# Optimization experiments

Measured on AMD Instinct MI355X. Metric: run time of the kernel, lower is better.

Reference implementation:

```python
import jax, jax.numpy as jnp
import numpy as np

B, S, D, H = 4, 4096, 1024, 16
DH = D // H  # 64
EPS = 1e-6


def setup_inputs() -> dict:
    key = jax.random.key(0)
    ks = jax.random.split(key, 6)
    scale = 1.0 / np.sqrt(D).astype(np.float32)
    x = jax.random.normal(ks[0], (B, S, D), jnp.float32)
    # packed cache: rows 0..DH-1 = KV state S0, row DH = normalizer z0 (kept positive)
    state_cache = jax.random.uniform(ks[1], (B, H, DH + 1, DH), jnp.float32)
    Wq = jax.random.normal(ks[2], (D, D), jnp.float32) * scale
    Wk = jax.random.normal(ks[3], (D, D), jnp.float32) * scale
    Wv = jax.random.normal(ks[4], (D, D), jnp.float32) * scale
    Wo = jax.random.normal(ks[5], (D, D), jnp.float32) * scale
    return {"x": x, "state_cache": state_cache, "Wq": Wq, "Wk": Wk, "Wv": Wv, "Wo": Wo}


def reference(x, state_cache, Wq, Wk, Wv, Wo):
    b, s, d = x.shape
    h, dh = H, d // H

    def heads(t):  # [b,s,d] -> [s,b,h,dh] (seq-major for scan)
        return t.reshape(b, s, h, dh).transpose(1, 0, 2, 3)

    phi = lambda t: jax.nn.elu(t) + 1.0  # positive feature map
    q = phi(heads(x @ Wq))
    k = phi(heads(x @ Wk))
    v = heads(x @ Wv)

    S0 = state_cache[:, :, :dh, :]   # [b,h,dh,dh]
    z0 = state_cache[:, :, dh, :]    # [b,h,dh]

    def step(carry, inp):
        Sst, z = carry
        qt, kt, vt = inp  # each [b,h,dh]
        Sst = Sst + jnp.einsum('bhd,bhe->bhde', kt, vt)
        z = z + kt
        num = jnp.einsum('bhd,bhde->bhe', qt, Sst)            # [b,h,dh]
        den = jnp.einsum('bhd,bhd->bh', qt, z)[..., None]     # [b,h,1]
        return (Sst, z), num / (den + EPS)

    _, outs = jax.lax.scan(step, (S0, z0), (q, k, v))  # outs: [s,b,h,dh]
    out = outs.transpose(1, 0, 2, 3).reshape(b, s, d)
    return out @ Wo
```

## Files before the change

kernel.cpp:

```cpp
#include <hip/hip_runtime.h>

#define B_ 4
#define S_ 4096
#define D_ 1024
#define H_ 16
#define DH 64
#define CHUNK 64
#define NC (S_ / CHUNK)
#define BH (B_ * H_)
#define STATE_N 4160
#define EPS 1e-6f

typedef __bf16 bf16;
typedef __bf16 bf16x8 __attribute__((ext_vector_type(8)));
typedef __bf16 bf16x4 __attribute__((ext_vector_type(4)));
typedef float v4f __attribute__((ext_vector_type(4)));

#define MFMA16(a, b, c) __builtin_amdgcn_mfma_f32_16x16x32_bf16(a, b, c, 0, 0, 0)

__device__ __forceinline__ void load_lds16(const bf16* g, bf16* l) {
  __builtin_amdgcn_global_load_lds(
      (const __attribute__((address_space(1))) unsigned int*)g,
      (__attribute__((address_space(3))) unsigned int*)l, 16, 0, 0);
}

__global__ __launch_bounds__(256) void cvt_f32_bf16(const float* __restrict__ in,
                                                    bf16* __restrict__ out) {
  const size_t i = ((size_t)blockIdx.x * 256 + threadIdx.x) * 8;
  float4 a = *(const float4*)(in + i);
  float4 b = *(const float4*)(in + i + 4);
  bf16x8 o;
  o[0] = (bf16)a.x; o[1] = (bf16)a.y; o[2] = (bf16)a.z; o[3] = (bf16)a.w;
  o[4] = (bf16)b.x; o[5] = (bf16)b.y; o[6] = (bf16)b.z; o[7] = (bf16)b.w;
  *(bf16x8*)(out + i) = o;
}

__global__ __launch_bounds__(256) void transpose_w4(
    const float* __restrict__ w0, const float* __restrict__ w1,
    const float* __restrict__ w2, const float* __restrict__ w3,
    bf16* __restrict__ out) {
  __shared__ float tile[32][33];
  const int z = blockIdx.z;
  const float* in = (z == 0) ? w0 : (z == 1) ? w1 : (z == 2) ? w2 : w3;
  bf16* o = out + (size_t)z * D_ * D_;
  const int bx = blockIdx.x * 32, by = blockIdx.y * 32;
  const int tx = threadIdx.x & 31, ty = threadIdx.x >> 5;
#pragma unroll
  for (int i = 0; i < 32; i += 8)
    tile[ty + i][tx] = in[(size_t)(by + ty + i) * D_ + bx + tx];
  __syncthreads();
#pragma unroll
  for (int i = 0; i < 32; i += 8)
    o[(size_t)(bx + ty + i) * D_ + by + tx] = (bf16)tile[tx][ty + i];
}

__global__ __launch_bounds__(256) void gemm_nt(const bf16* __restrict__ A,
                                               const bf16* __restrict__ BT,
                                               bf16* __restrict__ o0,
                                               bf16* __restrict__ o1,
                                               bf16* __restrict__ o2,
                                               float* __restrict__ of) {
  constexpr int TM = 128, BK = 32;
  constexpr int CLD = 132;
  __shared__ __align__(16) char smem[32768];
  float* Cl = (float*)smem;

  const int tid = threadIdx.x;
  const int wave = tid >> 6, lane = tid & 63;
  const int quad = lane >> 4, l16 = lane & 15;
  const int bm = blockIdx.x * TM;
  const int zz = blockIdx.y >> 3;
  const int colg = (blockIdx.y & 7) * 128;
  const int wm = (wave & 1) * 64, wn = (wave >> 1) * 64;
  const int act = (of == nullptr) && (zz < 2);
  bf16* ob = (zz == 0) ? o0 : (zz == 1) ? o1 : o2;

  const int srow = wave * 16 + (lane >> 2);
  const int sgrp = ((lane & 3) - ((lane >> 2) >> 1)) & 3;
  const bf16* gA0 = A + (size_t)(bm + srow) * D_ + sgrp * 8;
  const bf16* gA1 = gA0 + (size_t)64 * D_;
  const bf16* gB0 = BT + ((size_t)blockIdx.y * 128 + srow) * D_ + sgrp * 8;
  const bf16* gB1 = gB0 + (size_t)64 * D_;

  int offA[4], offB[4];
#pragma unroll
  for (int i = 0; i < 4; i++) {
    const int pg = (quad + (l16 >> 1)) & 3;
    offA[i] = (wm + i * 16 + l16) * BK + pg * 8;
    offB[i] = (wn + i * 16 + l16) * BK + pg * 8;
  }

  v4f zero = {0.f, 0.f, 0.f, 0.f};
  v4f acc[4][4];
#pragma unroll
  for (int i = 0; i < 4; i++)
#pragma unroll
    for (int j = 0; j < 4; j++) acc[i][j] = zero;

  auto stage = [&](int ks, int s) {
    bf16* As = (bf16*)(smem + s * 16384);
    bf16* Bs = As + 4096;
    const int ko = ks * BK;
    load_lds16(gA0 + ko, As + wave * 16 * BK);
    load_lds16(gA1 + ko, As + (64 + wave * 16) * BK);
    load_lds16(gB0 + ko, Bs + wave * 16 * BK);
    load_lds16(gB1 + ko, Bs + (64 + wave * 16) * BK);
  };
  auto compute = [&](int s) {
    const bf16* As = (const bf16*)(smem + s * 16384);
    const bf16* Bs = As + 4096;
    bf16x8 af[4], bfr[4];
#pragma unroll
    for (int i = 0; i < 4; i++) af[i] = *(const bf16x8*)&As[offA[i]];
#pragma unroll
    for (int j = 0; j < 4; j++) bfr[j] = *(const bf16x8*)&Bs[offB[j]];
#pragma unroll
    for (int i = 0; i < 4; i++)
#pragma unroll
      for (int j = 0; j < 4; j++) acc[i][j] = MFMA16(af[i], bfr[j], acc[i][j]);
  };

  constexpr int NK = D_ / BK;
  stage(0, 0);
  __syncthreads();
  for (int k = 0; k < NK; k += 2) {
    if (k + 1 < NK) stage(k + 1, 1);
    compute(0);
    __syncthreads();
    if (k + 2 < NK) stage(k + 2, 0);
    compute(1);
    __syncthreads();
  }

  const int lr = (wave & 1) * 16 + quad * 4;
  const int rrow = tid >> 3;
  const int rseg = (tid & 7) * 16;
  const int grow = bm + (rrow >> 4) * 64 + (rrow & 15);
#pragma unroll
  for (int i = 0; i < 4; i++) {
    __syncthreads();
#pragma unroll
    for (int j = 0; j < 4; j++) {
      const int col = wn + j * 16 + l16;
#pragma unroll
      for (int r = 0; r < 4; r++) {
        float x = acc[i][j][r];
        if (act) x = x > 0.f ? x + 1.f : __expf(x);
        Cl[(lr + r) * CLD + col] = x;
      }
    }
    __syncthreads();
    const float* src = &Cl[rrow * CLD + rseg];
    if (of) {
      float* dst = of + (size_t)(grow + i * 16) * D_ + colg + rseg;
#pragma unroll
      for (int u = 0; u < 4; u++)
        *(float4*)(dst + u * 4) = *(const float4*)(src + u * 4);
    } else {
      bf16x8 q0, q1;
#pragma unroll
      for (int u = 0; u < 8; u++) { q0[u] = (bf16)src[u]; q1[u] = (bf16)src[8 + u]; }
      bf16* dst = ob + (size_t)(grow + i * 16) * D_ + colg + rseg;
      *(bf16x8*)dst = q0;
      *(bf16x8*)(dst + 8) = q1;
    }
  }
}

__global__ __launch_bounds__(256) void chunk_kv(const bf16* __restrict__ kb,
                                                const bf16* __restrict__ vb,
                                                float* __restrict__ states) {
  constexpr int LD = 88;
  __shared__ bf16 Kl[CHUNK * LD];
  __shared__ bf16 Vl[CHUNK * LD];
  const int tid = threadIdx.x;
  const int c = blockIdx.x, bh = blockIdx.y;
  const int b = bh >> 4, h = bh & 15;
  const size_t gbase = ((size_t)(b * S_ + c * CHUNK)) * D_ + h * DH;
#pragma unroll
  for (int rep = 0; rep < 2; rep++) {
    int flat = tid + rep * 256;
    int r = flat >> 3, sg = (flat & 7) * 8;
    *(bf16x8*)&Kl[r * LD + sg] = *(const bf16x8*)(kb + gbase + (size_t)r * D_ + sg);
    *(bf16x8*)&Vl[r * LD + sg] = *(const bf16x8*)(vb + gbase + (size_t)r * D_ + sg);
  }
  __syncthreads();
  const int d0 = (tid >> 4) * 4, e0 = (tid & 15) * 4;
  float acc[4][4] = {};
  for (int t = 0; t < CHUNK; t++) {
    bf16x4 k4 = *(const bf16x4*)&Kl[t * LD + d0];
    bf16x4 v4 = *(const bf16x4*)&Vl[t * LD + e0];
    float kf[4], vf[4];
#pragma unroll
    for (int i = 0; i < 4; i++) { kf[i] = (float)k4[i]; vf[i] = (float)v4[i]; }
#pragma unroll
    for (int i = 0; i < 4; i++)
#pragma unroll
      for (int j = 0; j < 4; j++) acc[i][j] += kf[i] * vf[j];
  }
  float* out = states + ((size_t)bh * NC + c) * STATE_N;
#pragma unroll
  for (int i = 0; i < 4; i++)
#pragma unroll
    for (int j = 0; j < 4; j++) out[(d0 + i) * 64 + (e0 + j)] = acc[i][j];
  if (tid < 64) {
    float zs = 0.f;
    for (int t = 0; t < CHUNK; t++) zs += (float)Kl[t * LD + tid];
    out[4096 + tid] = zs;
  }
}

__global__ __launch_bounds__(256) void state_prefix(const float* __restrict__ sc,
                                                    float* __restrict__ states,
                                                    bf16* __restrict__ stb) {
  const int bh = blockIdx.x;
  const int e = blockIdx.y * 256 + threadIdx.x;
  if (e >= STATE_N) return;
  const float* scb = sc + (size_t)bh * (DH + 1) * DH;
  float run = scb[e];
  float* p = states + (size_t)bh * NC * STATE_N + e;
  if (e < 4096) {
    bf16* q = stb + (size_t)bh * NC * 4096 + e;
    for (int c = 0; c < NC; c++) {
      float tmp = p[(size_t)c * STATE_N];
      q[(size_t)c * 4096] = (bf16)run;
      run += tmp;
    }
  } else {
    for (int c = 0; c < NC; c++) {
      float tmp = p[(size_t)c * STATE_N];
      p[(size_t)c * STATE_N] = run;
      run += tmp;
    }
  }
}

__global__ __launch_bounds__(256) void attn_pass2(
    const bf16* __restrict__ qb, const bf16* __restrict__ kb,
    const bf16* __restrict__ vb, const float* __restrict__ states,
    const bf16* __restrict__ stb, bf16* __restrict__ ao) {
  constexpr int LD = 88;
  __shared__ bf16 Ql[CHUNK * LD];
  __shared__ bf16 Kl[CHUNK * LD];
  __shared__ bf16 VT[DH * LD];
  __shared__ bf16 S0T[DH * LD];
  __shared__ bf16 Pl[CHUNK * LD];
  __shared__ float denl[CHUNK];
  __shared__ float z0l[DH];
  const int tid = threadIdx.x;
  const int wave = tid >> 6, lane = tid & 63;
  const int quad = lane >> 4, l16 = lane & 15;
  const int c = blockIdx.x, bh = blockIdx.y;
  const int b = bh >> 4, h = bh & 15;
  const size_t gbase = ((size_t)(b * S_ + c * CHUNK)) * D_ + h * DH;

#pragma unroll
  for (int rep = 0; rep < 2; rep++) {
    int flat = tid + rep * 256;
    int r = flat >> 3, sg = (flat & 7) * 8;
    *(bf16x8*)&Ql[r * LD + sg] = *(const bf16x8*)(qb + gbase + (size_t)r * D_ + sg);
    *(bf16x8*)&Kl[r * LD + sg] = *(const bf16x8*)(kb + gbase + (size_t)r * D_ + sg);
    bf16x8 vv = *(const bf16x8*)(vb + gbase + (size_t)r * D_ + sg);
#pragma unroll
    for (int u = 0; u < 8; u++) VT[(sg + u) * LD + r] = vv[u];
  }
  {
    const bf16* stb_c = stb + ((size_t)bh * NC + c) * 4096;
    const int f0 = tid * 16;
    const int col = f0 >> 6, row0 = f0 & 63;
    bf16x8 a0 = *(const bf16x8*)&stb_c[f0];
    bf16x8 a1 = *(const bf16x8*)&stb_c[f0 + 8];
#pragma unroll
    for (int u = 0; u < 8; u++) {
      S0T[(row0 + u) * LD + col] = a0[u];
      S0T[(row0 + 8 + u) * LD + col] = a1[u];
    }
  }
  const float* st = states + ((size_t)bh * NC + c) * STATE_N;
  if (tid < DH) z0l[tid] = st[4096 + tid];
  __syncthreads();

  v4f zero = {0.f, 0.f, 0.f, 0.f};
  v4f pacc[4];
#pragma unroll
  for (int j = 0; j < 4; j++) pacc[j] = zero;
#pragma unroll
  for (int ks = 0; ks < 2; ks++) {
    bf16x8 aq = *(const bf16x8*)&Ql[(wave * 16 + l16) * LD + ks * 32 + quad * 8];
#pragma unroll
    for (int j = 0; j < 4; j++) {
      bf16x8 bk = *(const bf16x8*)&Kl[(j * 16 + l16) * LD + ks * 32 + quad * 8];
      pacc[j] = MFMA16(aq, bk, pacc[j]);
    }
  }
  float rs[4] = {0.f, 0.f, 0.f, 0.f};
#pragma unroll
  for (int j = 0; j < 4; j++) {
#pragma unroll
    for (int r = 0; r < 4; r++) {
      int t = wave * 16 + quad * 4 + r;
      int col = j * 16 + l16;
      float p = (col <= t) ? pacc[j][r] : 0.f;
      Pl[t * LD + col] = (bf16)p;
      rs[r] += p;
    }
  }
#pragma unroll
  for (int m = 1; m < 16; m <<= 1)
#pragma unroll
    for (int r = 0; r < 4; r++) rs[r] += __shfl_xor(rs[r], m, 64);
  if (l16 == 0)
#pragma unroll
    for (int r = 0; r < 4; r++) denl[wave * 16 + quad * 4 + r] = rs[r];
  __syncthreads();
  if (tid < CHUNK) {
    float qz = 0.f;
    for (int d = 0; d < DH; d++) qz += (float)Ql[tid * LD + d] * z0l[d];
    denl[tid] += qz;
  }
  __syncthreads();

  v4f nacc[4];
#pragma unroll
  for (int j = 0; j < 4; j++) nacc[j] = zero;
#pragma unroll
  for (int ks = 0; ks < 2; ks++) {
    bf16x8 ap = *(const bf16x8*)&Pl[(wave * 16 + l16) * LD + ks * 32 + quad * 8];
#pragma unroll
    for (int j = 0; j < 4; j++) {
      bf16x8 bv = *(const bf16x8*)&VT[(j * 16 + l16) * LD + ks * 32 + quad * 8];
      nacc[j] = MFMA16(ap, bv, nacc[j]);
    }
  }
#pragma unroll
  for (int ks = 0; ks < 2; ks++) {
    bf16x8 aq = *(const bf16x8*)&Ql[(wave * 16 + l16) * LD + ks * 32 + quad * 8];
#pragma unroll
    for (int j = 0; j < 4; j++) {
      bf16x8 bs = *(const bf16x8*)&S0T[(j * 16 + l16) * LD + ks * 32 + quad * 8];
      nacc[j] = MFMA16(aq, bs, nacc[j]);
    }
  }
#pragma unroll
  for (int j = 0; j < 4; j++) {
#pragma unroll
    for (int r = 0; r < 4; r++) {
      int t = wave * 16 + quad * 4 + r;
      int e = j * 16 + l16;
      float o = nacc[j][r] / (denl[t] + EPS);
      ao[gbase + (size_t)t * D_ + e] = (bf16)o;
    }
  }
}

extern "C" void kernel_launch(void* const* d_in, const int* in_sizes, int n_in,
                              void* d_out, int out_size, void* d_ws, size_t ws_size,
                              hipStream_t stream) {
  const float* x  = (const float*)d_in[0];
  const float* sc = (const float*)d_in[1];
  const float* Wq = (const float*)d_in[2];
  const float* Wk = (const float*)d_in[3];
  const float* Wv = (const float*)d_in[4];
  const float* Wo = (const float*)d_in[5];
  float* out = (float*)d_out;

  const size_t MSZ = (size_t)B_ * S_ * D_;
  const size_t WSZ = (size_t)D_ * D_;
  bf16* xb = (bf16*)d_ws;
  bf16* qb = xb + MSZ;
  bf16* kb = qb + MSZ;
  bf16* vb = kb + MSZ;
  bf16* ao = vb + MSZ;
  bf16* wt = ao + MSZ;
  float* states = (float*)(wt + 4 * WSZ);
  bf16* stb = xb;

  cvt_f32_bf16<<<MSZ / (256 * 8), 256, 0, stream>>>(x, xb);
  transpose_w4<<<dim3(32, 32, 4), 256, 0, stream>>>(Wq, Wk, Wv, Wo, wt);

  gemm_nt<<<dim3(128, 24), 256, 0, stream>>>(xb, wt, qb, kb, vb, nullptr);

  chunk_kv<<<dim3(NC, BH), 256, 0, stream>>>(kb, vb, states);
  state_prefix<<<dim3(BH, 17), 256, 0, stream>>>(sc, states, stb);
  attn_pass2<<<dim3(NC, BH), 256, 0, stream>>>(qb, kb, vb, states, stb, ao);

  gemm_nt<<<dim3(128, 8), 256, 0, stream>>>(ao, wt + 3 * WSZ, nullptr, nullptr,
                                            nullptr, out);
}
```

Baseline: 419.4 us.

## Use MFMA for chunk KV outer-product sum and parallelize reductions

The per-chunk K^T V state computation moves from scalar FMA outer products to bf16 MFMA. K and V are transposed into LDS so the time axis becomes the contraction dimension. The k-sum and q·z0 reductions now spread across all 256 threads with vector LDS loads and shuffles, replacing the 64-thread serial loops. The state prefix scan is hand-unrolled by four to batch its loads. The transposed scalar LDS stores may cause bank conflicts.

```diff
diff --git a/kernel.cpp b/kernel.cpp
--- a/kernel.cpp
+++ b/kernel.cpp
@@ -170,10 +170,12 @@
 __global__ __launch_bounds__(256) void chunk_kv(const bf16* __restrict__ kb,
                                                 const bf16* __restrict__ vb,
                                                 float* __restrict__ states) {
-  constexpr int LD = 88;
-  __shared__ bf16 Kl[CHUNK * LD];
-  __shared__ bf16 Vl[CHUNK * LD];
+  constexpr int LD = 72;
+  __shared__ bf16 KT[DH * LD];
+  __shared__ bf16 VT[DH * LD];
   const int tid = threadIdx.x;
+  const int wave = tid >> 6, lane = tid & 63;
+  const int quad = lane >> 4, l16 = lane & 15;
   const int c = blockIdx.x, bh = blockIdx.y;
   const int b = bh >> 4, h = bh & 15;
   const size_t gbase = ((size_t)(b * S_ + c * CHUNK)) * D_ + h * DH;
@@ -181,32 +183,46 @@
   for (int rep = 0; rep < 2; rep++) {
     int flat = tid + rep * 256;
     int r = flat >> 3, sg = (flat & 7) * 8;
-    *(bf16x8*)&Kl[r * LD + sg] = *(const bf16x8*)(kb + gbase + (size_t)r * D_ + sg);
-    *(bf16x8*)&Vl[r * LD + sg] = *(const bf16x8*)(vb + gbase + (size_t)r * D_ + sg);
-  }
-  __syncthreads();
-  const int d0 = (tid >> 4) * 4, e0 = (tid & 15) * 4;
-  float acc[4][4] = {};
-  for (int t = 0; t < CHUNK; t++) {
-    bf16x4 k4 = *(const bf16x4*)&Kl[t * LD + d0];
-    bf16x4 v4 = *(const bf16x4*)&Vl[t * LD + e0];
-    float kf[4], vf[4];
-#pragma unroll
-    for (int i = 0; i < 4; i++) { kf[i] = (float)k4[i]; vf[i] = (float)v4[i]; }
-#pragma unroll
-    for (int i = 0; i < 4; i++)
-#pragma unroll
-      for (int j = 0; j < 4; j++) acc[i][j] += kf[i] * vf[j];
+    bf16x8 kk = *(const bf16x8*)(kb + gbase + (size_t)r * D_ + sg);
+    bf16x8 vv = *(const bf16x8*)(vb + gbase + (size_t)r * D_ + sg);
+#pragma unroll
+    for (int u = 0; u < 8; u++) {
+      KT[(sg + u) * LD + r] = kk[u];
+      VT[(sg + u) * LD + r] = vv[u];
+    }
+  }
+  __syncthreads();
+
+  v4f zero = {0.f, 0.f, 0.f, 0.f};
+  v4f acc[4];
+#pragma unroll
+  for (int j = 0; j < 4; j++) acc[j] = zero;
+#pragma unroll
+  for (int ks = 0; ks < 2; ks++) {
+    bf16x8 ak = *(const bf16x8*)&KT[(wave * 16 + l16) * LD + ks * 32 + quad * 8];
+#pragma unroll
+    for (int j = 0; j < 4; j++) {
+      bf16x8 bv = *(const bf16x8*)&VT[(j * 16 + l16) * LD + ks * 32 + quad * 8];
+      acc[j] = MFMA16(ak, bv, acc[j]);
+    }
   }
   float* out = states + ((size_t)bh * NC + c) * STATE_N;
 #pragma unroll
-  for (int i = 0; i < 4; i++)
-#pragma unroll
-    for (int j = 0; j < 4; j++) out[(d0 + i) * 64 + (e0 + j)] = acc[i][j];
-  if (tid < 64) {
-    float zs = 0.f;
-    for (int t = 0; t < CHUNK; t++) zs += (float)Kl[t * LD + tid];
-    out[4096 + tid] = zs;
+  for (int j = 0; j < 4; j++)
+#pragma unroll
+    for (int r = 0; r < 4; r++)
+      out[(wave * 16 + quad * 4 + r) * 64 + (j * 16 + l16)] = acc[j][r];
+
+  {
+    const int d = tid >> 2, p = tid & 3;
+    bf16x8 a0 = *(const bf16x8*)&KT[d * LD + p * 16];
+    bf16x8 a1 = *(const bf16x8*)&KT[d * LD + p * 16 + 8];
+    float zp = 0.f;
+#pragma unroll
+    for (int u = 0; u < 8; u++) zp += (float)a0[u] + (float)a1[u];
+    zp += __shfl_xor(zp, 1, 64);
+    zp += __shfl_xor(zp, 2, 64);
+    if (p == 0) out[4096 + d] = zp;
   }
 }
 
@@ -221,16 +237,28 @@
   float* p = states + (size_t)bh * NC * STATE_N + e;
   if (e < 4096) {
     bf16* q = stb + (size_t)bh * NC * 4096 + e;
-    for (int c = 0; c < NC; c++) {
-      float tmp = p[(size_t)c * STATE_N];
-      q[(size_t)c * 4096] = (bf16)run;
-      run += tmp;
+#pragma unroll 1
+    for (int c = 0; c < NC; c += 4) {
+      float t0 = p[(size_t)(c + 0) * STATE_N];
+      float t1 = p[(size_t)(c + 1) * STATE_N];
+      float t2 = p[(size_t)(c + 2) * STATE_N];
+      float t3 = p[(size_t)(c + 3) * STATE_N];
+      q[(size_t)(c + 0) * 4096] = (bf16)run; run += t0;
+      q[(size_t)(c + 1) * 4096] = (bf16)run; run += t1;
+      q[(size_t)(c + 2) * 4096] = (bf16)run; run += t2;
+      q[(size_t)(c + 3) * 4096] = (bf16)run; run += t3;
     }
   } else {
-    for (int c = 0; c < NC; c++) {
-      float tmp = p[(size_t)c * STATE_N];
-      p[(size_t)c * STATE_N] = run;
-      run += tmp;
+#pragma unroll 1
+    for (int c = 0; c < NC; c += 4) {
+      float t0 = p[(size_t)(c + 0) * STATE_N];
+      float t1 = p[(size_t)(c + 1) * STATE_N];
+      float t2 = p[(size_t)(c + 2) * STATE_N];
+      float t3 = p[(size_t)(c + 3) * STATE_N];
+      p[(size_t)(c + 0) * STATE_N] = run; run += t0;
+      p[(size_t)(c + 1) * STATE_N] = run; run += t1;
+      p[(size_t)(c + 2) * STATE_N] = run; run += t2;
+      p[(size_t)(c + 3) * STATE_N] = run; run += t3;
     }
   }
 }
@@ -313,10 +341,17 @@
 #pragma unroll
     for (int r = 0; r < 4; r++) denl[wave * 16 + quad * 4 + r] = rs[r];
   __syncthreads();
-  if (tid < CHUNK) {
+  {
+    const int t = tid >> 2, p = tid & 3;
+    bf16x8 qa = *(const bf16x8*)&Ql[t * LD + p * 16];
+    bf16x8 qb2 = *(const bf16x8*)&Ql[t * LD + p * 16 + 8];
     float qz = 0.f;
-    for (int d = 0; d < DH; d++) qz += (float)Ql[tid * LD + d] * z0l[d];
-    denl[tid] += qz;
+#pragma unroll
+    for (int u = 0; u < 8; u++)
+      qz += (float)qa[u] * z0l[p * 16 + u] + (float)qb2[u] * z0l[p * 16 + 8 + u];
+    qz += __shfl_xor(qz, 1, 64);
+    qz += __shfl_xor(qz, 2, 64);
+    if (p == 0) denl[t] += qz;
   }
   __syncthreads();
 
```

Measured after the change: 415.5 us. Within noise of the previous version (-0.9%).
